# Kernel tuning notes

Hardware: AMD Instinct MI355X
Metric: run time of the kernel (lower is better)

## Reference

```python
import jax, jax.numpy as jnp
import numpy as np
from jax import lax

D_IN = 512     # input_dim
H_DIM = 1024   # hidden_dim
N_BATCH = 1024
T_STEPS = 64


def setup_inputs() -> dict:
    key = jax.random.key(0)
    ks = jax.random.split(key, 6)
    x = jax.random.normal(ks[0], (N_BATCH, T_STEPS, D_IN), dtype=jnp.float32)
    A = jax.random.normal(ks[1], (N_BATCH, H_DIM, 4, 4), dtype=jnp.float32)
    # parameters, init as in torch module
    Wx = jax.random.normal(ks[2], (D_IN, 4 * H_DIM), dtype=jnp.float32) / np.sqrt(D_IN)
    Wh = jax.random.normal(ks[3], (H_DIM, 4 * H_DIM), dtype=jnp.float32) / np.sqrt(H_DIM)
    Wattn = jax.random.normal(ks[4], (H_DIM, 4 * H_DIM), dtype=jnp.float32) / np.sqrt(H_DIM)
    b = jnp.zeros((4 * H_DIM,), dtype=jnp.float32)
    return {"x": x, "A": A, "Wx": Wx, "Wh": Wh, "Wattn": Wattn, "b": b}


def reference(x, A, Wx, Wh, Wattn, b):
    N, T, D = x.shape
    H = A.shape[1]
    Af = A.reshape(N, H, 16)              # (N, H, 16) flattened 4x4 grid
    h0 = Af.mean(axis=-1)                 # mean over spatial grid == mean(dim=(2,3))
    scale = 1.0 / jnp.sqrt(jnp.asarray(H, dtype=x.dtype))

    def step(carry, xt):
        h, c = carry
        # scaled dot-product attention over the 16 grid cells
        scores = jnp.einsum('nh,nhl->nl', h, Af) * scale   # (N, 16)
        w = jax.nn.softmax(scores, axis=-1)
        attn = jnp.einsum('nhl,nl->nh', Af, w)             # (N, H)
        a = xt @ Wx + h @ Wh + attn @ Wattn + b            # (N, 4H)
        ai, af, ao, ag = jnp.split(a, 4, axis=-1)
        i = jax.nn.sigmoid(ai)
        f = jax.nn.sigmoid(af)
        o = jax.nn.sigmoid(ao)
        g = jnp.tanh(ag)
        c_next = f * c + i * g
        h_next = o * jnp.tanh(c_next)
        return (h_next, c_next), h_next

    _, hs = lax.scan(step, (h0, h0), jnp.swapaxes(x, 0, 1))  # hs: (T, N, H)
    return jnp.swapaxes(hs, 0, 1)                            # (N, T, H)
```

## Files before the change

### kernel.cpp

```cpp
#include <hip/hip_runtime.h>
#include <cstdint>

#define NB    1024
#define TT    64
#define DIN   512
#define HD    1024
#define FH    4096
#define KTOT  2560

typedef _Float16 half8 __attribute__((ext_vector_type(8)));
typedef float floatx4 __attribute__((ext_vector_type(4)));

#define OFF_WT    ((size_t)0)
#define OFF_X16   ((size_t)20971520)
#define OFF_A16   ((size_t)88080384)
#define OFF_H16   ((size_t)121634816)
#define OFF_AT16  ((size_t)123731968)
#define OFF_HF    ((size_t)125829120)
#define OFF_C     ((size_t)130023424)
#define OFF_ABUF  ((size_t)134217728)

__device__ __forceinline__ void async_copy16(const void* g, void* l) {
    __builtin_amdgcn_global_load_lds(
        (const __attribute__((address_space(1))) void*)(uintptr_t)g,
        (__attribute__((address_space(3))) void*)(uintptr_t)l,
        16, 0, 0);
}

__global__ void k_convert_w(const float* __restrict__ Wx, const float* __restrict__ Wh,
                            const float* __restrict__ Wattn, _Float16* __restrict__ Wt) {
    __shared__ float tile[32][33];
    const int k0 = blockIdx.x * 32;
    const int c0 = blockIdx.y * 32;
    const int tx = threadIdx.x & 31;
    const int ty = threadIdx.x >> 5;
    const float* src; int kb;
    if (k0 < 512)       { src = Wx;    kb = k0; }
    else if (k0 < 1536) { src = Wh;    kb = k0 - 512; }
    else                { src = Wattn; kb = k0 - 1536; }
    #pragma unroll
    for (int r = ty; r < 32; r += 8)
        tile[r][tx] = src[(size_t)(kb + r) * FH + c0 + tx];
    __syncthreads();
    #pragma unroll
    for (int r = ty; r < 32; r += 8)
        Wt[(size_t)(c0 + r) * KTOT + k0 + tx] = (_Float16)tile[tx][r];
}

__global__ void k_convert(const float* __restrict__ src, _Float16* __restrict__ dst) {
    const size_t i = ((size_t)blockIdx.x * 256 + threadIdx.x) * 8;
    float4 v0 = *(const float4*)(src + i);
    float4 v1 = *(const float4*)(src + i + 4);
    half8 h;
    h[0] = (_Float16)v0.x; h[1] = (_Float16)v0.y; h[2] = (_Float16)v0.z; h[3] = (_Float16)v0.w;
    h[4] = (_Float16)v1.x; h[5] = (_Float16)v1.y; h[6] = (_Float16)v1.z; h[7] = (_Float16)v1.w;
    *(half8*)(dst + i) = h;
}

__global__ void k_init(const float* __restrict__ A, float* __restrict__ hf,
                       _Float16* __restrict__ h16, float* __restrict__ c) {
    const int idx = blockIdx.x * 256 + threadIdx.x;
    const float* a = A + (size_t)idx * 16;
    float s = 0.f;
    #pragma unroll
    for (int l = 0; l < 16; l++) s += a[l];
    const float m = s * (1.0f / 16.0f);
    hf[idx] = m; h16[idx] = (_Float16)m; c[idx] = m;
}

__device__ __forceinline__ void attn_phase(const _Float16* __restrict__ A16, int n,
                                           const float* hs ,
                                           float red[4][16] ,
                                           _Float16* __restrict__ at16) {
    const int tid = threadIdx.x, lane = tid & 63, wid = tid >> 6;
    float s[16];
    #pragma unroll
    for (int l = 0; l < 16; l++) s[l] = 0.f;
    half8 a0[4], a1[4];
    #pragma unroll
    for (int kk = 0; kk < 4; kk++) {
        const int r = kk * 256 + tid;
        const _Float16* ap = A16 + ((size_t)n * HD + r) * 16;
        a0[kk] = *(const half8*)ap;
        a1[kk] = *(const half8*)(ap + 8);
        const float hv = hs[r];
        #pragma unroll
        for (int l = 0; l < 8; l++) {
            s[l]     += hv * (float)a0[kk][l];
            s[l + 8] += hv * (float)a1[kk][l];
        }
    }
    #pragma unroll
    for (int l = 0; l < 16; l++)
        #pragma unroll
        for (int off = 32; off > 0; off >>= 1) s[l] += __shfl_down(s[l], off, 64);
    if (lane == 0) {
        #pragma unroll
        for (int l = 0; l < 16; l++) red[wid][l] = s[l];
    }
    __syncthreads();
    float w[16]; float mx = -1e30f;
    #pragma unroll
    for (int l = 0; l < 16; l++) {
        w[l] = (red[0][l] + red[1][l] + red[2][l] + red[3][l]) * 0.03125f;
        mx = fmaxf(mx, w[l]);
    }
    float sum = 0.f;
    #pragma unroll
    for (int l = 0; l < 16; l++) { w[l] = __expf(w[l] - mx); sum += w[l]; }
    const float inv = 1.0f / sum;
    #pragma unroll
    for (int l = 0; l < 16; l++) w[l] *= inv;
    #pragma unroll
    for (int kk = 0; kk < 4; kk++) {
        const int r = kk * 256 + tid;
        float v = 0.f;
        #pragma unroll
        for (int l = 0; l < 8; l++) v += (float)a0[kk][l] * w[l] + (float)a1[kk][l] * w[l + 8];
        at16[(size_t)n * HD + r] = (_Float16)v;
    }
}

__global__ void k_attn_boot(const _Float16* __restrict__ A16, const float* __restrict__ hf,
                            _Float16* __restrict__ at16) {
    __shared__ float hs[HD];
    __shared__ float red[4][16];
    const int n = blockIdx.x, tid = threadIdx.x;
    #pragma unroll
    for (int kk = 0; kk < 4; kk++) {
        const int r = kk * 256 + tid;
        hs[r] = hf[(size_t)n * HD + r];
    }
    __syncthreads();
    attn_phase(A16, n, hs, red, at16);
}

__global__ void k_cellattn(const float* __restrict__ abuf, const float* __restrict__ b,
                           const _Float16* __restrict__ A16,
                           float* __restrict__ c, _Float16* __restrict__ h16,
                           _Float16* __restrict__ at16, float* __restrict__ out, int t) {
    __shared__ float hs[HD];
    __shared__ float red[4][16];
    const int n = blockIdx.x, tid = threadIdx.x;
    #pragma unroll
    for (int kk = 0; kk < 4; kk++) {
        const int j = kk * 256 + tid;
        const size_t base = (size_t)n * FH + j;
        const float ai = abuf[base]        + b[j];
        const float af = abuf[base + 1024] + b[j + 1024];
        const float ao = abuf[base + 2048] + b[j + 2048];
        const float ag = abuf[base + 3072] + b[j + 3072];
        const float ig = 1.0f / (1.0f + __expf(-ai));
        const float fg = 1.0f / (1.0f + __expf(-af));
        const float og = 1.0f / (1.0f + __expf(-ao));
        const float gg = tanhf(ag);
        const int idx = n * HD + j;
        const float cn = fg * c[idx] + ig * gg;
        c[idx] = cn;
        const float hn = og * tanhf(cn);
        hs[j] = hn;
        h16[idx] = (_Float16)hn;
        out[(size_t)n * (TT * HD) + (size_t)t * HD + j] = hn;
    }
    if (t == TT - 1) return;
    __syncthreads();
    attn_phase(A16, n, hs, red, at16);
}

__launch_bounds__(256)
__global__ void k_gemm(const _Float16* __restrict__ xh, const _Float16* __restrict__ h16,
                       const _Float16* __restrict__ at16, const _Float16* __restrict__ Wt,
                       float* __restrict__ abuf, int t) {
    __shared__ _Float16 As[2][2][128 * 32];
    __shared__ _Float16 Bs[2][2][128 * 32];
    const int tid  = threadIdx.x;
    const int lane = tid & 63;
    const int w    = tid >> 6;
    const int wm   = w >> 1, wn = w & 1;
    const int bm0  = blockIdx.x * 128;
    const int bn0  = blockIdx.y * 128;
    const int srow = lane >> 2;
    const int scol = (lane & 3) * 8;

    auto stage = [&](int kb, int pp) {
        const _Float16* abase; int astride, klocal;
        if (kb < DIN)           { abase = xh + (size_t)t * DIN; astride = TT * DIN; klocal = kb; }
        else if (kb < DIN + HD) { abase = h16;  astride = HD; klocal = kb - DIN; }
        else                    { abase = at16; astride = HD; klocal = kb - DIN - HD; }
        #pragma unroll
        for (int s = 0; s < 2; s++) {
            #pragma unroll
            for (int q = 0; q < 2; q++) {
                const int row = w * 32 + q * 16 + srow;
                async_copy16(abase + (size_t)(bm0 + row) * astride + klocal + s * 32 + scol,
                             &As[pp][s][(w * 32 + q * 16) * 32]);
                async_copy16(Wt + (size_t)(bn0 + row) * KTOT + kb + s * 32 + scol,
                             &Bs[pp][s][(w * 32 + q * 16) * 32]);
            }
        }
    };

    floatx4 acc[4][4];
    #pragma unroll
    for (int i = 0; i < 4; i++)
        #pragma unroll
        for (int j = 0; j < 4; j++) acc[i][j] = (floatx4)0.0f;

    stage(0, 0);
    const int kq = (lane >> 4) * 8;
    const int rr = lane & 15;
    for (int it = 0; it < KTOT / 64; it++) {
        const int p = it & 1;
        __syncthreads();
        if (it < KTOT / 64 - 1) stage((it + 1) * 64, p ^ 1);
        #pragma unroll
        for (int s = 0; s < 2; s++) {
            half8 af[4], bf[4];
            #pragma unroll
            for (int i = 0; i < 4; i++)
                af[i] = *(const half8*)&As[p][s][(wm * 64 + i * 16 + rr) * 32 + kq];
            #pragma unroll
            for (int j = 0; j < 4; j++)
                bf[j] = *(const half8*)&Bs[p][s][(wn * 64 + j * 16 + rr) * 32 + kq];
            #pragma unroll
            for (int i = 0; i < 4; i++)
                #pragma unroll
                for (int j = 0; j < 4; j++)
                    acc[i][j] = __builtin_amdgcn_mfma_f32_16x16x32_f16(af[i], bf[j], acc[i][j], 0, 0, 0);
        }
    }
    const int q4 = (lane >> 4) * 4;
    const int cn = lane & 15;
    #pragma unroll
    for (int i = 0; i < 4; i++)
        #pragma unroll
        for (int j = 0; j < 4; j++)
            #pragma unroll
            for (int r = 0; r < 4; r++) {
                const int row = bm0 + wm * 64 + i * 16 + q4 + r;
                const int col = bn0 + wn * 64 + j * 16 + cn;
                abuf[(size_t)row * FH + col] = acc[i][j][r];
            }
}

extern "C" void kernel_launch(void* const* d_in, const int* in_sizes, int n_in,
                              void* d_out, int out_size, void* d_ws, size_t ws_size,
                              hipStream_t stream) {
    const float* x     = (const float*)d_in[0];
    const float* A     = (const float*)d_in[1];
    const float* Wx    = (const float*)d_in[2];
    const float* Wh    = (const float*)d_in[3];
    const float* Wattn = (const float*)d_in[4];
    const float* b     = (const float*)d_in[5];
    float* out = (float*)d_out;

    uint8_t* ws = (uint8_t*)d_ws;
    _Float16* Wt   = (_Float16*)(ws + OFF_WT);
    _Float16* x16  = (_Float16*)(ws + OFF_X16);
    _Float16* A16  = (_Float16*)(ws + OFF_A16);
    _Float16* h16  = (_Float16*)(ws + OFF_H16);
    _Float16* at16 = (_Float16*)(ws + OFF_AT16);
    float*    hf   = (float*)(ws + OFF_HF);
    float*    c    = (float*)(ws + OFF_C);
    float*    abuf = (float*)(ws + OFF_ABUF);

    k_convert_w<<<dim3(KTOT / 32, FH / 32), 256, 0, stream>>>(Wx, Wh, Wattn, Wt);
    k_convert<<<(NB * TT * DIN) / 2048, 256, 0, stream>>>(x, x16);
    k_convert<<<(NB * HD * 16) / 2048, 256, 0, stream>>>(A, A16);
    k_init<<<(NB * HD) / 256, 256, 0, stream>>>(A, hf, h16, c);
    k_attn_boot<<<NB, 256, 0, stream>>>(A16, hf, at16);

    for (int t = 0; t < TT; t++) {
        k_gemm<<<dim3(NB / 128, FH / 128), 256, 0, stream>>>(x16, h16, at16, Wt, abuf, t);
        k_cellattn<<<NB, 256, 0, stream>>>(abuf, b, A16, c, h16, at16, out, t);
    }
}
```

Measured before the change: 4.016 ms.

## Use 128x64 GEMM tiles with split-K across wave pairs and XCD-aware block mapping

The per-step GEMM tile shrinks from 128x128 to 128x64, doubling the grid to 512 blocks so more CUs are busy on the MI355X. Within a block, the two wave pairs each take one 32-wide K half and combine their partial sums through LDS at the end. Block IDs are remapped so each XCD works on a contiguous range of N columns, which should improve L2 reuse of the weights. The cost is extra A-tile loads per output, an LDS reduction step, and only half the waves doing the epilogue stores.

```diff
diff --git a/kernel.cpp b/kernel.cpp
--- a/kernel.cpp
+++ b/kernel.cpp
@@ -172,31 +172,38 @@
                        const _Float16* __restrict__ at16, const _Float16* __restrict__ Wt,
                        float* __restrict__ abuf, int t) {
     __shared__ _Float16 As[2][2][128 * 32];
-    __shared__ _Float16 Bs[2][2][128 * 32];
+    __shared__ _Float16 Bs[2][2][64 * 32];
     const int tid  = threadIdx.x;
     const int lane = tid & 63;
     const int w    = tid >> 6;
-    const int wm   = w >> 1, wn = w & 1;
-    const int bm0  = blockIdx.x * 128;
-    const int bn0  = blockIdx.y * 128;
+    const int g    = w >> 1;
+    const int wm   = w & 1;
+    const int bid = blockIdx.x;
+    const int xcd = bid & 7;
+    const int jj  = bid >> 3;
+    const int bm0 = (jj & 7) * 128;
+    const int bn0 = (xcd * 8 + (jj >> 3)) * 64;
     const int srow = lane >> 2;
     const int scol = (lane & 3) * 8;
 
-    auto stage = [&](int kb, int pp) {
-        const _Float16* abase; int astride, klocal;
-        if (kb < DIN)           { abase = xh + (size_t)t * DIN; astride = TT * DIN; klocal = kb; }
-        else if (kb < DIN + HD) { abase = h16;  astride = HD; klocal = kb - DIN; }
-        else                    { abase = at16; astride = HD; klocal = kb - DIN - HD; }
+    auto stage = [&](int it2) {
+        const int p  = it2 & 1;
+        const int kb = it2 * 64;
         #pragma unroll
         for (int s = 0; s < 2; s++) {
+            const int k0 = kb + s * 32;
+            const _Float16* abase; int astride, klocal;
+            if (k0 < DIN)           { abase = xh + (size_t)t * DIN; astride = TT * DIN; klocal = k0; }
+            else if (k0 < DIN + HD) { abase = h16;  astride = HD; klocal = k0 - DIN; }
+            else                    { abase = at16; astride = HD; klocal = k0 - DIN - HD; }
             #pragma unroll
             for (int q = 0; q < 2; q++) {
-                const int row = w * 32 + q * 16 + srow;
-                async_copy16(abase + (size_t)(bm0 + row) * astride + klocal + s * 32 + scol,
-                             &As[pp][s][(w * 32 + q * 16) * 32]);
-                async_copy16(Wt + (size_t)(bn0 + row) * KTOT + kb + s * 32 + scol,
-                             &Bs[pp][s][(w * 32 + q * 16) * 32]);
+                const int row = w * 32 + q * 16;
+                async_copy16(abase + (size_t)(bm0 + row + srow) * astride + klocal + scol,
+                             &As[p][s][row * 32]);
             }
+            async_copy16(Wt + (size_t)(bn0 + w * 16 + srow) * KTOT + k0 + scol,
+                         &Bs[p][s][(w * 16) * 32]);
         }
     };
 
@@ -206,41 +213,56 @@
         #pragma unroll
         for (int j = 0; j < 4; j++) acc[i][j] = (floatx4)0.0f;
 
-    stage(0, 0);
+    stage(0);
     const int kq = (lane >> 4) * 8;
     const int rr = lane & 15;
     for (int it = 0; it < KTOT / 64; it++) {
         const int p = it & 1;
         __syncthreads();
-        if (it < KTOT / 64 - 1) stage((it + 1) * 64, p ^ 1);
-        #pragma unroll
-        for (int s = 0; s < 2; s++) {
-            half8 af[4], bf[4];
-            #pragma unroll
-            for (int i = 0; i < 4; i++)
-                af[i] = *(const half8*)&As[p][s][(wm * 64 + i * 16 + rr) * 32 + kq];
-            #pragma unroll
-            for (int j = 0; j < 4; j++)
-                bf[j] = *(const half8*)&Bs[p][s][(wn * 64 + j * 16 + rr) * 32 + kq];
-            #pragma unroll
-            for (int i = 0; i < 4; i++)
+        if (it < KTOT / 64 - 1) stage(it + 1);
+        half8 af[4], bf[4];
+        #pragma unroll
+        for (int i = 0; i < 4; i++)
+            af[i] = *(const half8*)&As[p][g][(wm * 64 + i * 16 + rr) * 32 + kq];
+        #pragma unroll
+        for (int j = 0; j < 4; j++)
+            bf[j] = *(const half8*)&Bs[p][g][(j * 16 + rr) * 32 + kq];
+        #pragma unroll
+        for (int i = 0; i < 4; i++)
+            #pragma unroll
+            for (int j = 0; j < 4; j++)
+                acc[i][j] = __builtin_amdgcn_mfma_f32_16x16x32_f16(af[i], bf[j], acc[i][j], 0, 0, 0);
+    }
+
+    __syncthreads();
+    float* red = (float*)As;
+    if (g == 1) {
+        #pragma unroll
+        for (int i = 0; i < 4; i++)
+            #pragma unroll
+            for (int j = 0; j < 4; j++)
+                *(floatx4*)&red[((((wm * 4 + i) * 4 + j) * 64) + lane) * 4] = acc[i][j];
+    }
+    __syncthreads();
+    if (g == 0) {
+        #pragma unroll
+        for (int i = 0; i < 4; i++)
+            #pragma unroll
+            for (int j = 0; j < 4; j++)
+                acc[i][j] += *(const floatx4*)&red[((((wm * 4 + i) * 4 + j) * 64) + lane) * 4];
+        const int q4 = (lane >> 4) * 4;
+        const int cn = lane & 15;
+        #pragma unroll
+        for (int i = 0; i < 4; i++)
+            #pragma unroll
+            for (int j = 0; j < 4; j++)
                 #pragma unroll
-                for (int j = 0; j < 4; j++)
-                    acc[i][j] = __builtin_amdgcn_mfma_f32_16x16x32_f16(af[i], bf[j], acc[i][j], 0, 0, 0);
-        }
-    }
-    const int q4 = (lane >> 4) * 4;
-    const int cn = lane & 15;
-    #pragma unroll
-    for (int i = 0; i < 4; i++)
-        #pragma unroll
-        for (int j = 0; j < 4; j++)
-            #pragma unroll
-            for (int r = 0; r < 4; r++) {
-                const int row = bm0 + wm * 64 + i * 16 + q4 + r;
-                const int col = bn0 + wn * 64 + j * 16 + cn;
-                abuf[(size_t)row * FH + col] = acc[i][j][r];
-            }
+                for (int r = 0; r < 4; r++) {
+                    const int row = bm0 + wm * 64 + i * 16 + q4 + r;
+                    const int col = bn0 + j * 16 + cn;
+                    abuf[(size_t)row * FH + col] = acc[i][j][r];
+                }
+    }
 }
 
 extern "C" void kernel_launch(void* const* d_in, const int* in_sizes, int n_in,
@@ -271,7 +293,7 @@
     k_attn_boot<<<NB, 256, 0, stream>>>(A16, hf, at16);
 
     for (int t = 0; t < TT; t++) {
-        k_gemm<<<dim3(NB / 128, FH / 128), 256, 0, stream>>>(x16, h16, at16, Wt, abuf, t);
+        k_gemm<<<dim3(512), 256, 0, stream>>>(x16, h16, at16, Wt, abuf, t);
         k_cellattn<<<NB, 256, 0, stream>>>(abuf, b, A16, c, h16, at16, out, t);
     }
 }
```

New measurement: 3.516 ms. -12.5%, faster.
